# Kernel tuning notes

Hardware: AMD Instinct MI355X
Metric: run time of the kernel (lower is better)

Reference implementation:

```python
import jax, jax.numpy as jnp
import numpy as np

DIM = 1024
N_HEAD = 16
HEAD_DIM = DIM // N_HEAD
HIDDEN = 4 * DIM
EPS = 1e-6
NEG = -1e9


def setup_inputs() -> dict:
    key = jax.random.key(0)
    ks = jax.random.split(key, 9)
    B, T = 2, 2048
    x = jax.random.normal(ks[0], (B, T, DIM), dtype=jnp.float32)
    # additive causal mask [T, T]
    mask = jnp.where(jnp.tril(jnp.ones((T, T), dtype=bool)), 0.0, NEG).astype(jnp.float32)
    s = 0.02
    wq = jax.random.normal(ks[1], (DIM, DIM), dtype=jnp.float32) * s
    wk = jax.random.normal(ks[2], (DIM, DIM), dtype=jnp.float32) * s
    wv = jax.random.normal(ks[3], (DIM, DIM), dtype=jnp.float32) * s
    wo = jax.random.normal(ks[4], (DIM, DIM), dtype=jnp.float32) * s
    w1 = jax.random.normal(ks[5], (DIM, HIDDEN), dtype=jnp.float32) * s
    w2 = jax.random.normal(ks[6], (HIDDEN, DIM), dtype=jnp.float32) * s
    g_attn = jnp.ones((DIM,), dtype=jnp.float32)
    g_ffn = jnp.ones((DIM,), dtype=jnp.float32)
    return {"x": x, "mask": mask, "wq": wq, "wk": wk, "wv": wv, "wo": wo,
            "w1": w1, "w2": w2, "g_attn": g_attn, "g_ffn": g_ffn}


def _rmsnorm(x, g):
    norm = jax.lax.rsqrt(jnp.mean(jnp.square(x), axis=-1, keepdims=True) + EPS)
    return (x * norm) * g


def _attention(x, mask, wq, wk, wv, wo):
    B, T, C = x.shape
    # project and split heads: [B, H, T, D]
    q = (x @ wq).reshape(B, T, N_HEAD, HEAD_DIM).transpose(0, 2, 1, 3)
    k = (x @ wk).reshape(B, T, N_HEAD, HEAD_DIM).transpose(0, 2, 1, 3)
    v = (x @ wv).reshape(B, T, N_HEAD, HEAD_DIM).transpose(0, 2, 1, 3)
    attn = jnp.einsum('bhtd,bhsd->bhts', q, k) / np.sqrt(HEAD_DIM).astype(np.float32)
    attn = attn + mask  # broadcast [T,T] over [B,H,T,T]
    p = jax.nn.softmax(attn, axis=-1)
    out = jnp.einsum('bhts,bhsd->bhtd', p, v)
    out = out.transpose(0, 2, 1, 3).reshape(B, T, C)
    return out @ wo


def reference(x, mask, wq, wk, wv, wo, w1, w2, g_attn, g_ffn):
    x = x + _attention(_rmsnorm(x, g_attn), mask, wq, wk, wv, wo)
    h = _rmsnorm(x, g_ffn)
    return x + (jax.nn.silu(h @ w1) @ w2)
```

## Files before the change

kernel.cpp:

```cpp
#include <hip/hip_runtime.h>
#include <hip/hip_bf16.h>
#include <cstdint>
#include <cstddef>

#define DIM    1024
#define NHEAD  16
#define HDIM   64
#define HIDDEN 4096
#define TSEQ   2048
#define TOKENS 4096

typedef __attribute__((ext_vector_type(4))) float  f32x4;
typedef __attribute__((ext_vector_type(8))) short  short8;
typedef __attribute__((ext_vector_type(8))) __bf16 bf16x8;

__device__ __forceinline__ short f2bf(float f) {
    union { float f; uint32_t u; } v; v.f = f;
    uint32_t u = v.u;
    uint32_t r = (u + 0x7fffu + ((u >> 16) & 1u)) >> 16;
    return (short)r;
}

__device__ __forceinline__ float bf2f(short s) {
    uint32_t u = ((uint32_t)(uint16_t)s) << 16;
    return __builtin_bit_cast(float, u);
}

__device__ __forceinline__ f32x4 mfma_bf16(short8 a, short8 b, f32x4 c) {
    return __builtin_amdgcn_mfma_f32_16x16x32_bf16(
        __builtin_bit_cast(bf16x8, a), __builtin_bit_cast(bf16x8, b), c, 0, 0, 0);
}

__device__ __forceinline__ void barrier_lds() {
    asm volatile("s_waitcnt lgkmcnt(0)\n\ts_barrier" ::: "memory");
}

__global__ __launch_bounds__(256) void transpose_w(
    const float* __restrict__ W, short* __restrict__ Wt, int K, int N)
{
    __shared__ float tile[64][65];
    const int tid = threadIdx.x;
    const int n0 = blockIdx.x * 64, k0 = blockIdx.y * 64;
    for (int i = tid; i < 4096; i += 256) {
        int r = i >> 6, c = i & 63;
        tile[r][c] = W[(size_t)(k0 + r) * N + n0 + c];
    }
    __syncthreads();
    for (int i = tid; i < 4096; i += 256) {
        int r = i >> 6, c = i & 63;
        Wt[(size_t)(n0 + r) * K + k0 + c] = f2bf(tile[c][r]);
    }
}

__global__ __launch_bounds__(256) void transpose_v(
    const short* __restrict__ qkv, short* __restrict__ Vt)
{
    __shared__ short tile[64][72];
    const int tid = threadIdx.x;
    const int s0 = blockIdx.x * 64, bh = blockIdx.y;
    const int b = bh >> 4, h = bh & 15;
    const short* src = qkv + ((size_t)(b * TSEQ + s0)) * 3072 + 2048 + h * 64;
    for (int i = tid; i < 512; i += 256) {
        int r = i >> 3, cg = i & 7;
        *(short8*)&tile[r][cg * 8] = *(const short8*)(src + (size_t)r * 3072 + cg * 8);
    }
    __syncthreads();
    short* dst = Vt + ((size_t)bh * 64) * TSEQ + s0;
    for (int i = tid; i < 512; i += 256) {
        int d = i >> 3, sg = i & 7;
        short8 o;
#pragma unroll
        for (int j = 0; j < 8; ++j) o[j] = tile[sg * 8 + j][d];
        *(short8*)(dst + (size_t)d * TSEQ + sg * 8) = o;
    }
}

__global__ __launch_bounds__(256) void rmsnorm_k(
    const float* __restrict__ x, const float* __restrict__ g, short* __restrict__ out)
{
    const int t = blockIdx.x, tid = threadIdx.x;
    const int wave = tid >> 6, lane = tid & 63;
    const float4 v = ((const float4*)(x + (size_t)t * DIM))[tid];
    float ss = v.x * v.x + v.y * v.y + v.z * v.z + v.w * v.w;
#pragma unroll
    for (int d = 1; d < 64; d <<= 1) ss += __shfl_xor(ss, d, 64);
    __shared__ float red[4];
    if (lane == 0) red[wave] = ss;
    __syncthreads();
    float tot = red[0] + red[1] + red[2] + red[3];
    float rn = rsqrtf(tot * (1.0f / (float)DIM) + 1e-6f);
    const float4 gv = ((const float4*)g)[tid];
    short4 ov = make_short4(f2bf(v.x * rn * gv.x), f2bf(v.y * rn * gv.y),
                            f2bf(v.z * rn * gv.z), f2bf(v.w * rn * gv.w));
    ((short4*)(out + (size_t)t * DIM))[tid] = ov;
}

template <int EPI>
__global__ __launch_bounds__(256) void gemm_bt(
    const short* __restrict__ A, const short* __restrict__ Bt,
    void* __restrict__ Cout, const float* __restrict__ res,
    int M, int N, int K)
{
    __shared__ short As[128 * 32];
    __shared__ short Bs[128 * 32];
    const int tid  = threadIdx.x;
    const int wave = tid >> 6, lane = tid & 63;
    const int lm = lane & 15, quad = lane >> 4;
    const int wm = wave & 1, wn = wave >> 1;
    const int m0 = blockIdx.x * 128, n0 = blockIdx.y * 128;
    const int Ksl = K / gridDim.z;
    const int kbeg = blockIdx.z * Ksl;
    const int nIter = Ksl >> 5;

    const f32x4 zero = {0.f, 0.f, 0.f, 0.f};
    f32x4 acc[4][4];
#pragma unroll
    for (int i = 0; i < 4; ++i)
#pragma unroll
        for (int j = 0; j < 4; ++j) acc[i][j] = zero;

    const int lrow = wave * 32 + (lane >> 2);
    const int lcol = (lane & 3) * 8;
    const short* Ap = A + (size_t)(m0 + lrow) * K + kbeg + lcol;
    const short* Bp = Bt + (size_t)(n0 + lrow) * K + kbeg + lcol;
    const int woff = lrow * 32 + lcol;

    short8 a00, a01, b00, b01;
    short8 a10, a11, b10, b11;

    auto compute = [&]() {
        short8 af[4], bf[4];
#pragma unroll
        for (int mt = 0; mt < 4; ++mt)
            af[mt] = *(const short8*)&As[(wm * 64 + mt * 16 + lm) * 32 + quad * 8];
#pragma unroll
        for (int nt = 0; nt < 4; ++nt)
            bf[nt] = *(const short8*)&Bs[(wn * 64 + nt * 16 + lm) * 32 + quad * 8];
#pragma unroll
        for (int mt = 0; mt < 4; ++mt)
#pragma unroll
            for (int nt = 0; nt < 4; ++nt)
                acc[mt][nt] = mfma_bf16(af[mt], bf[nt], acc[mt][nt]);
    };

    a00 = *(const short8*)Ap;  a01 = *(const short8*)(Ap + (size_t)16 * K);
    b00 = *(const short8*)Bp;  b01 = *(const short8*)(Bp + (size_t)16 * K);
    Ap += 32; Bp += 32;
    a10 = *(const short8*)Ap;  a11 = *(const short8*)(Ap + (size_t)16 * K);
    b10 = *(const short8*)Bp;  b11 = *(const short8*)(Bp + (size_t)16 * K);
    Ap += 32; Bp += 32;

    for (int it = 0; it < nIter; it += 2) {
        barrier_lds();
        *(short8*)&As[woff] = a00;
        *(short8*)&As[woff + 512] = a01;
        *(short8*)&Bs[woff] = b00;
        *(short8*)&Bs[woff + 512] = b01;
        barrier_lds();
        if (it + 2 < nIter) {
            a00 = *(const short8*)Ap;  a01 = *(const short8*)(Ap + (size_t)16 * K);
            b00 = *(const short8*)Bp;  b01 = *(const short8*)(Bp + (size_t)16 * K);
            Ap += 32; Bp += 32;
        }
        compute();
        barrier_lds();
        *(short8*)&As[woff] = a10;
        *(short8*)&As[woff + 512] = a11;
        *(short8*)&Bs[woff] = b10;
        *(short8*)&Bs[woff + 512] = b11;
        barrier_lds();
        if (it + 3 < nIter) {
            a10 = *(const short8*)Ap;  a11 = *(const short8*)(Ap + (size_t)16 * K);
            b10 = *(const short8*)Bp;  b11 = *(const short8*)(Bp + (size_t)16 * K);
            Ap += 32; Bp += 32;
        }
        compute();
    }

#pragma unroll
    for (int mt = 0; mt < 4; ++mt) {
#pragma unroll
        for (int r = 0; r < 4; ++r) {
            const int row = m0 + wm * 64 + mt * 16 + quad * 4 + r;
#pragma unroll
            for (int nt = 0; nt < 4; ++nt) {
                const int col = n0 + wn * 64 + nt * 16 + lm;
                const size_t idx = (size_t)row * N + col;
                const float v = acc[mt][nt][r];
                if constexpr (EPI == 0) {
                    ((short*)Cout)[idx] = f2bf(v);
                } else if constexpr (EPI == 1) {
                    ((float*)Cout)[idx] = res[idx] + v;
                } else if constexpr (EPI == 2) {
                    ((short*)Cout)[idx] = f2bf(v / (1.0f + __expf(-v)));
                } else {
                    ((short*)Cout)[(size_t)blockIdx.z * M * N + idx] = f2bf(v);
                }
            }
        }
    }
}

__global__ __launch_bounds__(256) void combine_k4(
    const short* __restrict__ p, const float* __restrict__ res,
    float* __restrict__ out, int n)
{
    const int i = blockIdx.x * 256 + threadIdx.x;
    if (i * 4 < n) {
        float4 v = ((const float4*)res)[i];
#pragma unroll
        for (int s = 0; s < 4; ++s) {
            short4 ps = ((const short4*)(p + (size_t)s * n))[i];
            v.x += bf2f(ps.x); v.y += bf2f(ps.y);
            v.z += bf2f(ps.z); v.w += bf2f(ps.w);
        }
        ((float4*)out)[i] = v;
    }
}

__global__ __launch_bounds__(256) void combine_rms4(
    const short* __restrict__ p, const float* __restrict__ res,
    const float* __restrict__ g, float* __restrict__ x2out,
    short* __restrict__ nout)
{
    const int t = blockIdx.x, tid = threadIdx.x;
    const int wave = tid >> 6, lane = tid & 63;
    const size_t i4 = (size_t)t * 256 + tid;
    float4 v = ((const float4*)res)[i4];
#pragma unroll
    for (int s = 0; s < 4; ++s) {
        short4 ps = ((const short4*)(p + (size_t)s * TOKENS * DIM))[i4];
        v.x += bf2f(ps.x); v.y += bf2f(ps.y);
        v.z += bf2f(ps.z); v.w += bf2f(ps.w);
    }
    ((float4*)x2out)[i4] = v;
    float ss = v.x * v.x + v.y * v.y + v.z * v.z + v.w * v.w;
#pragma unroll
    for (int d = 1; d < 64; d <<= 1) ss += __shfl_xor(ss, d, 64);
    __shared__ float red[4];
    if (lane == 0) red[wave] = ss;
    __syncthreads();
    float tot = red[0] + red[1] + red[2] + red[3];
    float rn = rsqrtf(tot * (1.0f / (float)DIM) + 1e-6f);
    const float4 gv = ((const float4*)g)[tid];
    short4 ov = make_short4(f2bf(v.x * rn * gv.x), f2bf(v.y * rn * gv.y),
                            f2bf(v.z * rn * gv.z), f2bf(v.w * rn * gv.w));
    ((short4*)nout)[i4] = ov;
}

#define LP 72
__global__ __launch_bounds__(128) void attn_k(
    const short* __restrict__ qkv, const short* __restrict__ Vt,
    short* __restrict__ out)
{
    __shared__ short Qs[64 * LP];
    __shared__ short Ks[64 * LP];
    __shared__ short Vts[64 * LP];
    __shared__ short Ps[2][32 * LP];

    const int tid = threadIdx.x, wave = tid >> 6, lane = tid & 63;
    const int lm = lane & 15, quad = lane >> 4;
    const int bh = blockIdx.x;
    const int qt = (gridDim.y - 1) - blockIdx.y;
    const int b = bh >> 4, h = bh & 15;
    const int q0 = qt * 64;

    const int rr = tid >> 3, cg = tid & 7;

    const short* qbase = qkv + ((size_t)(b * TSEQ + q0)) * 3072 + h * 64;
#pragma unroll
    for (int j = 0; j < 4; ++j)
        *(short8*)&Qs[(rr + j * 16) * LP + cg * 8] =
            *(const short8*)(qbase + (size_t)(rr + j * 16) * 3072 + cg * 8);

    const short* kb  = qkv + (size_t)b * TSEQ * 3072 + 1024 + h * 64;
    const short* vtb = Vt + (size_t)bh * 64 * TSEQ;

    short8 kr[4], vr[4];
#pragma unroll
    for (int j = 0; j < 4; ++j) {
        kr[j] = *(const short8*)(kb + (size_t)(rr + j * 16) * 3072 + cg * 8);
        vr[j] = *(const short8*)(vtb + (size_t)(rr + j * 16) * TSEQ + cg * 8);
    }

    const f32x4 zero = {0.f, 0.f, 0.f, 0.f};
    f32x4 o_acc[2][4];
#pragma unroll
    for (int mt = 0; mt < 2; ++mt)
#pragma unroll
        for (int t = 0; t < 4; ++t) o_acc[mt][t] = zero;
    float lsum[2][4] = {{0.f, 0.f, 0.f, 0.f}, {0.f, 0.f, 0.f, 0.f}};

    for (int st = 0; st <= qt; ++st) {
        __syncthreads();
#pragma unroll
        for (int j = 0; j < 4; ++j) {
            *(short8*)&Ks[(rr + j * 16) * LP + cg * 8] = kr[j];
            *(short8*)&Vts[(rr + j * 16) * LP + cg * 8] = vr[j];
        }
        __syncthreads();
        if (st < qt) {
            const size_t sn = (size_t)(st + 1) * 64;
#pragma unroll
            for (int j = 0; j < 4; ++j) {
                kr[j] = *(const short8*)(kb + (sn + rr + j * 16) * 3072 + cg * 8);
                vr[j] = *(const short8*)(vtb + (size_t)(rr + j * 16) * TSEQ + sn + cg * 8);
            }
        }

        f32x4 sa[2][4];
#pragma unroll
        for (int mt = 0; mt < 2; ++mt)
#pragma unroll
            for (int nt = 0; nt < 4; ++nt) sa[mt][nt] = zero;
#pragma unroll
        for (int kk = 0; kk < 2; ++kk) {
            short8 aq0 = *(const short8*)&Qs[(wave * 32 + lm) * LP + kk * 32 + quad * 8];
            short8 aq1 = *(const short8*)&Qs[(wave * 32 + 16 + lm) * LP + kk * 32 + quad * 8];
#pragma unroll
            for (int nt = 0; nt < 4; ++nt) {
                short8 bk = *(const short8*)&Ks[(nt * 16 + lm) * LP + kk * 32 + quad * 8];
                sa[0][nt] = mfma_bf16(aq0, bk, sa[0][nt]);
                sa[1][nt] = mfma_bf16(aq1, bk, sa[1][nt]);
            }
        }

        const int s0 = st * 64;
        const bool band = (st == qt);
#pragma unroll
        for (int mt = 0; mt < 2; ++mt) {
            const int qrow = q0 + wave * 32 + mt * 16 + quad * 4;
#pragma unroll
            for (int nt = 0; nt < 4; ++nt) {
                const int col = s0 + nt * 16 + lm;
#pragma unroll
                for (int r = 0; r < 4; ++r) {
                    float p = __expf(0.125f * sa[mt][nt][r]);
                    if (band && col > qrow + r) p = 0.f;
                    lsum[mt][r] += p;
                    Ps[wave][(mt * 16 + quad * 4 + r) * LP + nt * 16 + lm] =
                        (short)(__builtin_bit_cast(uint32_t, p) >> 16);
                }
            }
        }

#pragma unroll
        for (int kk = 0; kk < 2; ++kk) {
            short8 ap0 = *(const short8*)&Ps[wave][lm * LP + kk * 32 + quad * 8];
            short8 ap1 = *(const short8*)&Ps[wave][(16 + lm) * LP + kk * 32 + quad * 8];
#pragma unroll
            for (int t = 0; t < 4; ++t) {
                short8 bv = *(const short8*)&Vts[(t * 16 + lm) * LP + kk * 32 + quad * 8];
                o_acc[0][t] = mfma_bf16(ap0, bv, o_acc[0][t]);
                o_acc[1][t] = mfma_bf16(ap1, bv, o_acc[1][t]);
            }
        }
    }

#pragma unroll
    for (int mt = 0; mt < 2; ++mt)
#pragma unroll
        for (int r = 0; r < 4; ++r) {
            float s = lsum[mt][r];
#pragma unroll
            for (int d = 1; d < 16; d <<= 1) s += __shfl_xor(s, d, 16);
            lsum[mt][r] = s;
        }

#pragma unroll
    for (int mt = 0; mt < 2; ++mt)
#pragma unroll
        for (int r = 0; r < 4; ++r) {
            const float inv = 1.0f / lsum[mt][r];
            const int token = b * TSEQ + q0 + wave * 32 + mt * 16 + quad * 4 + r;
#pragma unroll
            for (int t = 0; t < 4; ++t)
                out[(size_t)token * 1024 + h * 64 + t * 16 + lm] = f2bf(o_acc[mt][t][r] * inv);
        }
}

extern "C" void kernel_launch(void* const* d_in, const int* in_sizes, int n_in,
                              void* d_out, int out_size, void* d_ws, size_t ws_size,
                              hipStream_t stream)
{
    const float* x      = (const float*)d_in[0];
    const float* wq     = (const float*)d_in[2];
    const float* wk     = (const float*)d_in[3];
    const float* wv     = (const float*)d_in[4];
    const float* wo     = (const float*)d_in[5];
    const float* w1     = (const float*)d_in[6];
    const float* w2     = (const float*)d_in[7];
    const float* g_attn = (const float*)d_in[8];
    const float* g_ffn  = (const float*)d_in[9];
    float* out = (float*)d_out;

    char* ws = (char*)d_ws;
    const size_t MB = 1024 * 1024;
    short* Wqkv_t = (short*)(ws + 0);
    short* Wo_t   = (short*)(ws + 6 * MB);
    short* W1_t   = (short*)(ws + 8 * MB);
    short* xn     = (short*)(ws + 16 * MB);
    short* hbuf   = (short*)(ws + 24 * MB);
    short* qkv    = (short*)(ws + 32 * MB);
    short* pbufO  = (short*)(ws + 32 * MB);
    short* Vt     = (short*)(ws + 64 * MB);
    float* x2     = (float*)(ws + 64 * MB);
    short* W2_t   = (short*)(ws + 80 * MB);
    short* pbuf2  = (short*)(ws + 0);

    dim3 blk(256);

    transpose_w<<<dim3(16, 16), blk, 0, stream>>>(wq, Wqkv_t, 1024, 1024);
    transpose_w<<<dim3(16, 16), blk, 0, stream>>>(wk, Wqkv_t + (size_t)1024 * 1024, 1024, 1024);
    transpose_w<<<dim3(16, 16), blk, 0, stream>>>(wv, Wqkv_t + (size_t)2048 * 1024, 1024, 1024);
    transpose_w<<<dim3(16, 16), blk, 0, stream>>>(wo, Wo_t, 1024, 1024);
    transpose_w<<<dim3(64, 16), blk, 0, stream>>>(w1, W1_t, 1024, 4096);
    transpose_w<<<dim3(16, 64), blk, 0, stream>>>(w2, W2_t, 4096, 1024);

    rmsnorm_k<<<TOKENS, blk, 0, stream>>>(x, g_attn, xn);

    gemm_bt<0><<<dim3(TOKENS / 128, 3072 / 128), blk, 0, stream>>>(
        xn, Wqkv_t, qkv, nullptr, TOKENS, 3072, 1024);

    transpose_v<<<dim3(TSEQ / 64, 32), blk, 0, stream>>>(qkv, Vt);

    attn_k<<<dim3(32, TSEQ / 64), dim3(128), 0, stream>>>(qkv, Vt, xn);

    gemm_bt<3><<<dim3(TOKENS / 128, 1024 / 128, 4), blk, 0, stream>>>(
        xn, Wo_t, pbufO, nullptr, TOKENS, 1024, 1024);

    combine_rms4<<<TOKENS, blk, 0, stream>>>(pbufO, x, g_ffn, x2, hbuf);

    gemm_bt<2><<<dim3(TOKENS / 128, HIDDEN / 128), blk, 0, stream>>>(
        hbuf, W1_t, qkv, nullptr, TOKENS, HIDDEN, 1024);

    gemm_bt<3><<<dim3(TOKENS / 128, 1024 / 128, 4), blk, 0, stream>>>(
        qkv, W2_t, pbuf2, nullptr, TOKENS, 1024, HIDDEN);

    combine_k4<<<dim3(TOKENS * DIM / 4 / 256), blk, 0, stream>>>(
        pbuf2, x2, out, TOKENS * DIM);
}
```

Before: 367.1 us.

## Load Q/K/V MFMA fragments directly from global into registers, dropping LDS staging

The attention kernel no longer stages Q, K and V^T tiles through shared memory. Each wave loads its MFMA operand fragments straight from global memory into registers, double-buffers the K fragments across a two-step unrolled loop, and loads V fragments at the start of each step. This removes two __syncthreads per KV step and shrinks LDS use, and launch bounds now ask for 2 blocks per SIMD. The cost is that both waves fetch the same K/V fragments redundantly (relying on cache), the loads are less coalesced, V load latency is exposed within each step, and register pressure goes up.

```diff
diff --git a/kernel.cpp b/kernel.cpp
--- a/kernel.cpp
+++ b/kernel.cpp
@@ -249,13 +249,10 @@
 }
 
 #define LP 72
-__global__ __launch_bounds__(128) void attn_k(
+__global__ __launch_bounds__(128, 2) void attn_k(
     const short* __restrict__ qkv, const short* __restrict__ Vt,
     short* __restrict__ out)
 {
-    __shared__ short Qs[64 * LP];
-    __shared__ short Ks[64 * LP];
-    __shared__ short Vts[64 * LP];
     __shared__ short Ps[2][32 * LP];
 
     const int tid = threadIdx.x, wave = tid >> 6, lane = tid & 63;
@@ -265,24 +262,17 @@
     const int b = bh >> 4, h = bh & 15;
     const int q0 = qt * 64;
 
-    const int rr = tid >> 3, cg = tid & 7;
-
-    const short* qbase = qkv + ((size_t)(b * TSEQ + q0)) * 3072 + h * 64;
-#pragma unroll
-    for (int j = 0; j < 4; ++j)
-        *(short8*)&Qs[(rr + j * 16) * LP + cg * 8] =
-            *(const short8*)(qbase + (size_t)(rr + j * 16) * 3072 + cg * 8);
+    const short* qb = qkv + ((size_t)(b * TSEQ + q0)) * 3072 + h * 64;
+    short8 aq[2][2];
+#pragma unroll
+    for (int mt = 0; mt < 2; ++mt)
+#pragma unroll
+        for (int kk = 0; kk < 2; ++kk)
+            aq[mt][kk] = *(const short8*)(qb + (size_t)(wave * 32 + mt * 16 + lm) * 3072 + kk * 32 + quad * 8);
 
     const short* kb  = qkv + (size_t)b * TSEQ * 3072 + 1024 + h * 64;
     const short* vtb = Vt + (size_t)bh * 64 * TSEQ;
 
-    short8 kr[4], vr[4];
-#pragma unroll
-    for (int j = 0; j < 4; ++j) {
-        kr[j] = *(const short8*)(kb + (size_t)(rr + j * 16) * 3072 + cg * 8);
-        vr[j] = *(const short8*)(vtb + (size_t)(rr + j * 16) * TSEQ + cg * 8);
-    }
-
     const f32x4 zero = {0.f, 0.f, 0.f, 0.f};
     f32x4 o_acc[2][4];
 #pragma unroll
@@ -291,41 +281,44 @@
         for (int t = 0; t < 4; ++t) o_acc[mt][t] = zero;
     float lsum[2][4] = {{0.f, 0.f, 0.f, 0.f}, {0.f, 0.f, 0.f, 0.f}};
 
-    for (int st = 0; st <= qt; ++st) {
-        __syncthreads();
-#pragma unroll
-        for (int j = 0; j < 4; ++j) {
-            *(short8*)&Ks[(rr + j * 16) * LP + cg * 8] = kr[j];
-            *(short8*)&Vts[(rr + j * 16) * LP + cg * 8] = vr[j];
-        }
-        __syncthreads();
+    short8 kA[8], kB[8];
+#pragma unroll
+    for (int nt = 0; nt < 4; ++nt)
+#pragma unroll
+        for (int kk = 0; kk < 2; ++kk)
+            kA[nt * 2 + kk] = *(const short8*)(kb + (size_t)(nt * 16 + lm) * 3072 + kk * 32 + quad * 8);
+
+    auto body = [&](short8 (&kc)[8], short8 (&kn)[8], const int st) {
+        const int s0 = st * 64;
+
+        short8 vf[8];
+#pragma unroll
+        for (int t = 0; t < 4; ++t)
+#pragma unroll
+            for (int kk = 0; kk < 2; ++kk)
+                vf[t * 2 + kk] = *(const short8*)(vtb + (size_t)(t * 16 + lm) * TSEQ + s0 + kk * 32 + quad * 8);
+
+        f32x4 sa[2][4];
+#pragma unroll
+        for (int mt = 0; mt < 2; ++mt)
+#pragma unroll
+            for (int nt = 0; nt < 4; ++nt) sa[mt][nt] = zero;
+#pragma unroll
+        for (int kk = 0; kk < 2; ++kk)
+#pragma unroll
+            for (int nt = 0; nt < 4; ++nt) {
+                sa[0][nt] = mfma_bf16(aq[0][kk], kc[nt * 2 + kk], sa[0][nt]);
+                sa[1][nt] = mfma_bf16(aq[1][kk], kc[nt * 2 + kk], sa[1][nt]);
+            }
+
         if (st < qt) {
-            const size_t sn = (size_t)(st + 1) * 64;
-#pragma unroll
-            for (int j = 0; j < 4; ++j) {
-                kr[j] = *(const short8*)(kb + (sn + rr + j * 16) * 3072 + cg * 8);
-                vr[j] = *(const short8*)(vtb + (size_t)(rr + j * 16) * TSEQ + sn + cg * 8);
-            }
-        }
-
-        f32x4 sa[2][4];
-#pragma unroll
-        for (int mt = 0; mt < 2; ++mt)
-#pragma unroll
-            for (int nt = 0; nt < 4; ++nt) sa[mt][nt] = zero;
-#pragma unroll
-        for (int kk = 0; kk < 2; ++kk) {
-            short8 aq0 = *(const short8*)&Qs[(wave * 32 + lm) * LP + kk * 32 + quad * 8];
-            short8 aq1 = *(const short8*)&Qs[(wave * 32 + 16 + lm) * LP + kk * 32 + quad * 8];
-#pragma unroll
-            for (int nt = 0; nt < 4; ++nt) {
-                short8 bk = *(const short8*)&Ks[(nt * 16 + lm) * LP + kk * 32 + quad * 8];
-                sa[0][nt] = mfma_bf16(aq0, bk, sa[0][nt]);
-                sa[1][nt] = mfma_bf16(aq1, bk, sa[1][nt]);
-            }
-        }
-
-        const int s0 = st * 64;
+#pragma unroll
+            for (int nt = 0; nt < 4; ++nt)
+#pragma unroll
+                for (int kk = 0; kk < 2; ++kk)
+                    kn[nt * 2 + kk] = *(const short8*)(kb + (size_t)(s0 + 64 + nt * 16 + lm) * 3072 + kk * 32 + quad * 8);
+        }
+
         const bool band = (st == qt);
 #pragma unroll
         for (int mt = 0; mt < 2; ++mt) {
@@ -350,12 +343,18 @@
             short8 ap1 = *(const short8*)&Ps[wave][(16 + lm) * LP + kk * 32 + quad * 8];
 #pragma unroll
             for (int t = 0; t < 4; ++t) {
-                short8 bv = *(const short8*)&Vts[(t * 16 + lm) * LP + kk * 32 + quad * 8];
-                o_acc[0][t] = mfma_bf16(ap0, bv, o_acc[0][t]);
-                o_acc[1][t] = mfma_bf16(ap1, bv, o_acc[1][t]);
+                o_acc[0][t] = mfma_bf16(ap0, vf[t * 2 + kk], o_acc[0][t]);
+                o_acc[1][t] = mfma_bf16(ap1, vf[t * 2 + kk], o_acc[1][t]);
             }
         }
-    }
+    };
+
+    int st = 0;
+    for (; st + 1 <= qt; st += 2) {
+        body(kA, kB, st);
+        body(kB, kA, st + 1);
+    }
+    if (st <= qt) body(kA, kB, st);
 
 #pragma unroll
     for (int mt = 0; mt < 2; ++mt)
```

Result: slower. 403.0 us (+9.8%).

## Split attention KV range across two wave pairs and merge partial outputs

Applied to the files above, without the earlier changes.

The attention kernel goes from 128 to 256 threads. Two pairs of waves each process half of the causal key/value tiles, and the second pair's partial output and row sums are merged through shared memory. Q fragments are now held in registers instead of a shared tile. The goal is more parallelism per query tile, which shortens the long causal loops of late query tiles. The cost is extra shared memory, a final reduction step, and higher register pressure under launch_bounds(256,2).

```diff
diff --git a/kernel.cpp b/kernel.cpp
--- a/kernel.cpp
+++ b/kernel.cpp
@@ -249,40 +249,41 @@
 }
 
 #define LP 72
-__global__ __launch_bounds__(128) void attn_k(
+__global__ __launch_bounds__(256, 2) void attn_k(
     const short* __restrict__ qkv, const short* __restrict__ Vt,
     short* __restrict__ out)
 {
-    __shared__ short Qs[64 * LP];
-    __shared__ short Ks[64 * LP];
-    __shared__ short Vts[64 * LP];
-    __shared__ short Ps[2][32 * LP];
+    __shared__ short Ks[2][64 * LP];
+    __shared__ short Vts[2][64 * LP];
+    __shared__ short Ps[4][32 * LP];
 
     const int tid = threadIdx.x, wave = tid >> 6, lane = tid & 63;
+    const int pair = wave >> 1, wv = wave & 1;
     const int lm = lane & 15, quad = lane >> 4;
     const int bh = blockIdx.x;
     const int qt = (gridDim.y - 1) - blockIdx.y;
     const int b = bh >> 4, h = bh & 15;
     const int q0 = qt * 64;
 
-    const int rr = tid >> 3, cg = tid & 7;
-
-    const short* qbase = qkv + ((size_t)(b * TSEQ + q0)) * 3072 + h * 64;
-#pragma unroll
-    for (int j = 0; j < 4; ++j)
-        *(short8*)&Qs[(rr + j * 16) * LP + cg * 8] =
-            *(const short8*)(qbase + (size_t)(rr + j * 16) * 3072 + cg * 8);
+    const int n  = qt + 1;
+    const int nA = (n + 1) >> 1;
+    const int nP = pair ? (n >> 1) : nA;
+    const int sbase = pair ? nA : 0;
+
+    const int tp = tid & 127;
+    const int rr = tp >> 3, cg = tp & 7;
+
+    const short* qb = qkv + ((size_t)(b * TSEQ + q0)) * 3072 + h * 64;
+    short8 aq[2][2];
+#pragma unroll
+    for (int mt = 0; mt < 2; ++mt)
+#pragma unroll
+        for (int kk = 0; kk < 2; ++kk)
+            aq[mt][kk] = *(const short8*)(qb + (size_t)(wv * 32 + mt * 16 + lm) * 3072 + kk * 32 + quad * 8);
 
     const short* kb  = qkv + (size_t)b * TSEQ * 3072 + 1024 + h * 64;
     const short* vtb = Vt + (size_t)bh * 64 * TSEQ;
 
-    short8 kr[4], vr[4];
-#pragma unroll
-    for (int j = 0; j < 4; ++j) {
-        kr[j] = *(const short8*)(kb + (size_t)(rr + j * 16) * 3072 + cg * 8);
-        vr[j] = *(const short8*)(vtb + (size_t)(rr + j * 16) * TSEQ + cg * 8);
-    }
-
     const f32x4 zero = {0.f, 0.f, 0.f, 0.f};
     f32x4 o_acc[2][4];
 #pragma unroll
@@ -291,15 +292,29 @@
         for (int t = 0; t < 4; ++t) o_acc[mt][t] = zero;
     float lsum[2][4] = {{0.f, 0.f, 0.f, 0.f}, {0.f, 0.f, 0.f, 0.f}};
 
-    for (int st = 0; st <= qt; ++st) {
+    short8 kr[4], vr[4];
+    if (nP > 0) {
+        const size_t s0 = (size_t)sbase * 64;
+#pragma unroll
+        for (int j = 0; j < 4; ++j) {
+            kr[j] = *(const short8*)(kb + (s0 + rr + j * 16) * 3072 + cg * 8);
+            vr[j] = *(const short8*)(vtb + (size_t)(rr + j * 16) * TSEQ + s0 + cg * 8);
+        }
+    }
+
+    for (int it = 0; it < nA; ++it) {
+        const int st = sbase + it;
+        const bool act = it < nP;
         __syncthreads();
-#pragma unroll
-        for (int j = 0; j < 4; ++j) {
-            *(short8*)&Ks[(rr + j * 16) * LP + cg * 8] = kr[j];
-            *(short8*)&Vts[(rr + j * 16) * LP + cg * 8] = vr[j];
+        if (act) {
+#pragma unroll
+            for (int j = 0; j < 4; ++j) {
+                *(short8*)&Ks[pair][(rr + j * 16) * LP + cg * 8] = kr[j];
+                *(short8*)&Vts[pair][(rr + j * 16) * LP + cg * 8] = vr[j];
+            }
         }
         __syncthreads();
-        if (st < qt) {
+        if (act && it + 1 < nP) {
             const size_t sn = (size_t)(st + 1) * 64;
 #pragma unroll
             for (int j = 0; j < 4; ++j) {
@@ -307,6 +322,7 @@
                 vr[j] = *(const short8*)(vtb + (size_t)(rr + j * 16) * TSEQ + sn + cg * 8);
             }
         }
+        if (!act) continue;
 
         f32x4 sa[2][4];
 #pragma unroll
@@ -315,13 +331,11 @@
             for (int nt = 0; nt < 4; ++nt) sa[mt][nt] = zero;
 #pragma unroll
         for (int kk = 0; kk < 2; ++kk) {
-            short8 aq0 = *(const short8*)&Qs[(wave * 32 + lm) * LP + kk * 32 + quad * 8];
-            short8 aq1 = *(const short8*)&Qs[(wave * 32 + 16 + lm) * LP + kk * 32 + quad * 8];
 #pragma unroll
             for (int nt = 0; nt < 4; ++nt) {
-                short8 bk = *(const short8*)&Ks[(nt * 16 + lm) * LP + kk * 32 + quad * 8];
-                sa[0][nt] = mfma_bf16(aq0, bk, sa[0][nt]);
-                sa[1][nt] = mfma_bf16(aq1, bk, sa[1][nt]);
+                short8 bk = *(const short8*)&Ks[pair][(nt * 16 + lm) * LP + kk * 32 + quad * 8];
+                sa[0][nt] = mfma_bf16(aq[0][kk], bk, sa[0][nt]);
+                sa[1][nt] = mfma_bf16(aq[1][kk], bk, sa[1][nt]);
             }
         }
 
@@ -329,7 +343,7 @@
         const bool band = (st == qt);
 #pragma unroll
         for (int mt = 0; mt < 2; ++mt) {
-            const int qrow = q0 + wave * 32 + mt * 16 + quad * 4;
+            const int qrow = q0 + wv * 32 + mt * 16 + quad * 4;
 #pragma unroll
             for (int nt = 0; nt < 4; ++nt) {
                 const int col = s0 + nt * 16 + lm;
@@ -350,7 +364,7 @@
             short8 ap1 = *(const short8*)&Ps[wave][(16 + lm) * LP + kk * 32 + quad * 8];
 #pragma unroll
             for (int t = 0; t < 4; ++t) {
-                short8 bv = *(const short8*)&Vts[(t * 16 + lm) * LP + kk * 32 + quad * 8];
+                short8 bv = *(const short8*)&Vts[pair][(t * 16 + lm) * LP + kk * 32 + quad * 8];
                 o_acc[0][t] = mfma_bf16(ap0, bv, o_acc[0][t]);
                 o_acc[1][t] = mfma_bf16(ap1, bv, o_acc[1][t]);
             }
@@ -367,16 +381,43 @@
             lsum[mt][r] = s;
         }
 
-#pragma unroll
-    for (int mt = 0; mt < 2; ++mt)
-#pragma unroll
-        for (int r = 0; r < 4; ++r) {
-            const float inv = 1.0f / lsum[mt][r];
-            const int token = b * TSEQ + q0 + wave * 32 + mt * 16 + quad * 4 + r;
+    __syncthreads();
+    float* Ob = (float*)&Ks[0][0];
+    float* Lb = (float*)&Vts[0][0];
+    if (pair == 1) {
+#pragma unroll
+        for (int mt = 0; mt < 2; ++mt)
 #pragma unroll
             for (int t = 0; t < 4; ++t)
-                out[(size_t)token * 1024 + h * 64 + t * 16 + lm] = f2bf(o_acc[mt][t][r] * inv);
-        }
+#pragma unroll
+                for (int r = 0; r < 4; ++r)
+                    Ob[(wv * 32 + mt * 16 + quad * 4 + r) * 68 + t * 16 + lm] = o_acc[mt][t][r];
+        if (lm == 0) {
+#pragma unroll
+            for (int mt = 0; mt < 2; ++mt)
+#pragma unroll
+                for (int r = 0; r < 4; ++r)
+                    Lb[wv * 32 + mt * 16 + quad * 4 + r] = lsum[mt][r];
+        }
+    }
+    __syncthreads();
+    if (pair == 0) {
+#pragma unroll
+        for (int mt = 0; mt < 2; ++mt) {
+#pragma unroll
+            for (int r = 0; r < 4; ++r) {
+                const int lrow = wv * 32 + mt * 16 + quad * 4 + r;
+                float ltot = lsum[mt][r] + Lb[lrow];
+                const float inv = 1.0f / ltot;
+                const int token = b * TSEQ + q0 + lrow;
+#pragma unroll
+                for (int t = 0; t < 4; ++t) {
+                    float o = o_acc[mt][t][r] + Ob[lrow * 68 + t * 16 + lm];
+                    out[(size_t)token * 1024 + h * 64 + t * 16 + lm] = f2bf(o * inv);
+                }
+            }
+        }
+    }
 }
 
 extern "C" void kernel_launch(void* const* d_in, const int* in_sizes, int n_in,
@@ -424,7 +465,7 @@
 
     transpose_v<<<dim3(TSEQ / 64, 32), blk, 0, stream>>>(qkv, Vt);
 
-    attn_k<<<dim3(32, TSEQ / 64), dim3(128), 0, stream>>>(qkv, Vt, xn);
+    attn_k<<<dim3(32, TSEQ / 64), dim3(256), 0, stream>>>(qkv, Vt, xn);
 
     gemm_bt<3><<<dim3(TOKENS / 128, 1024 / 128, 4), blk, 0, stream>>>(
         xn, Wo_t, pbufO, nullptr, TOKENS, 1024, 1024);
```

New measurement: 370.3 us. Within noise of the previous version (+0.9%).
